# Optimization experiments

Hardware: AMD Instinct MI355X
Metric: run time of the kernel (lower is better)

Reference implementation:

```python
import jax, jax.numpy as jnp
import numpy as np

B, T, C = 2, 2048, 1024
H = 16
D = C // H  # head_dim = 64
EPS = 1e-06
MAX_SEQ = 2048


def make_rotary(dim, max_seq_len, base=10000):
    inv_freq = 1.0 / (base ** (jnp.arange(0, dim, 2, dtype=jnp.float32) / dim))
    pos = jnp.arange(max_seq_len, dtype=jnp.float32)
    sinusoid = jnp.einsum('i,j->ij', pos, inv_freq)  # (S, dim//2)
    return jnp.sin(sinusoid), jnp.cos(sinusoid)


def apply_rotary(x, sin, cos):
    # x: (B, T, H, D); sin/cos: (MAX_SEQ, D//2)
    t = x.shape[1]
    s = sin[:t][:, None, :]  # (T,1,D//2) broadcasts over B and H
    c = cos[:t][:, None, :]
    d = x.shape[-1]
    x1, x2 = x[..., :d // 2], x[..., d // 2:]
    return jnp.concatenate([x1 * c - x2 * s, x2 * c + x1 * s], axis=-1)


def yat_dense(x, kernel, bias, alpha, eps=EPS):
    # Yat layer: squared dot product over squared euclidean distance.
    dot = x @ kernel                                   # (..., out)
    x_sq = jnp.sum(x * x, axis=-1, keepdims=True)      # (..., 1)
    k_sq = jnp.sum(kernel * kernel, axis=0)            # (out,)
    dist = x_sq + k_sq - 2.0 * dot
    y = (dot * dot) / (dist + eps)
    out_f = kernel.shape[1]
    scale = (jnp.sqrt(jnp.float32(out_f)) / jnp.log(1.0 + jnp.float32(out_f))) ** alpha
    return y * scale + bias


def setup_inputs() -> dict:
    key = jax.random.key(0)
    ks = jax.random.split(key, 7)
    x = jax.random.normal(ks[0], (B, T, C), dtype=jnp.float32)
    mask = jnp.tril(jnp.ones((T, T), dtype=bool))[None].repeat(B, axis=0)  # (B,T,T) causal
    s = 1.0 / np.sqrt(C)
    w_attn = jax.random.normal(ks[1], (C, 3 * C), dtype=jnp.float32) * s
    b_attn = jnp.zeros((3 * C,), dtype=jnp.float32)
    a_attn = jnp.ones((1,), dtype=jnp.float32)
    w_proj = jax.random.normal(ks[2], (C, C), dtype=jnp.float32) * s
    b_proj = jnp.zeros((C,), dtype=jnp.float32)
    a_proj = jnp.ones((1,), dtype=jnp.float32)
    return {"x": x, "mask": mask, "w_attn": w_attn, "b_attn": b_attn,
            "a_attn": a_attn, "w_proj": w_proj, "b_proj": b_proj, "a_proj": a_proj}


def reference(x, mask, w_attn, b_attn, a_attn, w_proj, b_proj, a_proj):
    b, t, c = x.shape
    sin, cos = make_rotary(D, MAX_SEQ)
    qkv = yat_dense(x, w_attn, b_attn, a_attn)          # (B,T,3C)
    qkv = qkv.reshape(b, t, 3, H, D)
    q, k, v = jnp.moveaxis(qkv, 2, 0)                   # each (B,T,H,D)
    q = apply_rotary(q, sin, cos)
    k = apply_rotary(k, sin, cos)
    # heads-major layout for attention
    q = q.transpose(0, 2, 1, 3)                          # (B,H,T,D)
    k = k.transpose(0, 2, 1, 3)
    v = v.transpose(0, 2, 1, 3)
    scale = jnp.sqrt(jnp.float32(D))
    attn = jnp.einsum('bhqd,bhkd->bhqk', q, k) / scale   # (B,H,T,T)
    m = mask[:, None, :, :]                              # (B,1,T,T)
    attn = jnp.where(m, attn, jnp.finfo(jnp.float32).min)
    attn = jax.nn.softmax(attn, axis=-1)
    # dropout is identity in deterministic/eval mode
    out = jnp.einsum('bhqk,bhkd->bhqd', attn, v)         # (B,H,T,D)
    out = out.transpose(0, 2, 1, 3).reshape(b, t, c)     # (B,T,C)
    out = yat_dense(out, w_proj, b_proj, a_proj)
    return out
```

## Files before the change

### kernel.cpp

```cpp
#include <hip/hip_runtime.h>
#include <math.h>

#define TSEQ  2048
#define BATCH 2
#define NH    16
#define HD    64
#define CDIM  1024
#define N3C   3072
#define EPSY  1e-6f

typedef unsigned short u16;
typedef unsigned int u32;
typedef __attribute__((ext_vector_type(8))) short bf16x8;
typedef __attribute__((ext_vector_type(4))) float f32x4;

#define MFMA16(a, b, c) __builtin_amdgcn_mfma_f32_16x16x32_bf16(a, b, c, 0, 0, 0)

__device__ __forceinline__ u16 f2bf(float f) {
    unsigned u = __float_as_uint(f);
    return (u16)((u + 0x7fffu + ((u >> 16) & 1u)) >> 16);
}
__device__ __forceinline__ float bf2f(u16 h) {
    return __uint_as_float(((unsigned)h) << 16);
}
__device__ __forceinline__ void gload16(const void* g, void* l) {
    __builtin_amdgcn_global_load_lds(
        (const __attribute__((address_space(1))) unsigned int*)g,
        (__attribute__((address_space(3))) unsigned int*)l, 16, 0, 0);
}

__global__ void rope_init(float2* __restrict__ sc) {
    int idx = blockIdx.x * 256 + threadIdx.x;
    int t = idx >> 5, j = idx & 31;
    float inv = exp2f(-(float)j * 0.4152410118609203f);
    float ang = (float)t * inv;
    sc[idx] = make_float2(cosf(ang), sinf(ang));
}

__global__ void colsq_kernel(const float* __restrict__ wa,
                             const float* __restrict__ wp,
                             float* __restrict__ ks) {
    int bid = blockIdx.x, tid = threadIdx.x;
    int c = tid & 63, kq = tid >> 6;
    const float* W; int N, col, outoff;
    if (bid < 48) { W = wa; N = N3C;  col = bid * 64 + c;        outoff = 0;   }
    else          { W = wp; N = CDIM; col = (bid - 48) * 64 + c; outoff = N3C; }
    float s = 0.f;
    int i0 = kq * 256;
    #pragma unroll 4
    for (int i = i0; i < i0 + 256; ++i) {
        float v = W[(size_t)i * N + col];
        s = fmaf(v, v, s);
    }
    __shared__ float red[256];
    red[tid] = s;
    __syncthreads();
    if (kq == 0) ks[outoff + col] = red[c] + red[64 + c] + red[128 + c] + red[192 + c];
}

__global__ void convert_rows(const float* __restrict__ X, u16* __restrict__ Xhi,
                             float* __restrict__ rsq) {
    int row = blockIdx.x, tid = threadIdx.x;
    int lane = tid & 63, wv = tid >> 6;
    size_t base = (size_t)row * CDIM + tid * 4;
    float4 v = *(const float4*)(X + base);
    ushort4 hi;
    hi.x = f2bf(v.x); hi.y = f2bf(v.y); hi.z = f2bf(v.z); hi.w = f2bf(v.w);
    *(ushort4*)(Xhi + base) = hi;
    float s = v.x * v.x + v.y * v.y + v.z * v.z + v.w * v.w;
    #pragma unroll
    for (int off = 32; off; off >>= 1) s += __shfl_down(s, off, 64);
    __shared__ float red[4];
    if (lane == 0) red[wv] = s;
    __syncthreads();
    if (tid == 0) rsq[row] = red[0] + red[1] + red[2] + red[3];
}

__global__ void convert_wT(const float* __restrict__ W, u16* __restrict__ Whi,
                           int K, int N) {
    __shared__ float tile[64][68];
    int k0 = blockIdx.y * 64, n0 = blockIdx.x * 64;
    int tid = threadIdx.x;
    int r = tid >> 4, c4 = (tid & 15) * 4;
    #pragma unroll
    for (int i = 0; i < 4; ++i) {
        int k = k0 + r + i * 16;
        float4 v = *(const float4*)(W + (size_t)k * N + n0 + c4);
        *(float4*)&tile[r + i * 16][c4] = v;
    }
    __syncthreads();
    int n = tid >> 4, k4 = (tid & 15) * 4;
    #pragma unroll
    for (int i = 0; i < 4; ++i) {
        int nn = n + i * 16;
        ushort4 hi;
        hi.x = f2bf(tile[k4 + 0][nn]);
        hi.y = f2bf(tile[k4 + 1][nn]);
        hi.z = f2bf(tile[k4 + 2][nn]);
        hi.w = f2bf(tile[k4 + 3][nn]);
        *(ushort4*)(Whi + (size_t)(n0 + nn) * K + k0 + k4) = hi;
    }
}

__global__ __launch_bounds__(256, 4) void gemm1_fused(
    const u16* __restrict__ Ah, const u16* __restrict__ Bh,
    const float* __restrict__ bias, const float* __restrict__ rowsq,
    const float* __restrict__ colsq, const float* __restrict__ alphap,
    const float2* __restrict__ ropeSC,
    u16* __restrict__ Qb, u16* __restrict__ Kb, u16* __restrict__ Vt) {
    constexpr int BK = 32;
    const int K = CDIM;
    __shared__ u16 Ash[128 * BK], Bsh[128 * BK];
    int tid = threadIdx.x;
    int lane = tid & 63, wv = tid >> 6;
    int quad = lane >> 4, l15 = lane & 15;
    int wr = wv >> 1, wc = wv & 1;
    int bm = blockIdx.y * 128, bn = blockIdx.x * 128;
    int rsub = lane >> 2;
    int lc8 = (lane & 3) * 8;
    int gc8 = (((lane & 3) - (rsub >> 1)) & 3) * 8;
    int pf8 = ((quad + (l15 >> 1)) & 3) * 8;

    f32x4 acc[4][4];
    #pragma unroll
    for (int i = 0; i < 4; ++i)
        #pragma unroll
        for (int j = 0; j < 4; ++j) acc[i][j] = (f32x4){0.f, 0.f, 0.f, 0.f};

    for (int kt = 0; kt < K; kt += BK) {
        #pragma unroll
        for (int i = 0; i < 2; ++i) {
            int r = i * 64 + wv * 16 + rsub;
            gload16(Ah + (size_t)(bm + r) * K + kt + gc8, &Ash[r * BK + lc8]);
            gload16(Bh + (size_t)(bn + r) * K + kt + gc8, &Bsh[r * BK + lc8]);
        }
        __syncthreads();
        bf16x8 fah[4], fbh[4];
        #pragma unroll
        for (int i = 0; i < 4; ++i)
            fah[i] = *(const bf16x8*)&Ash[(wr * 64 + i * 16 + l15) * BK + pf8];
        #pragma unroll
        for (int j = 0; j < 4; ++j)
            fbh[j] = *(const bf16x8*)&Bsh[(wc * 64 + j * 16 + l15) * BK + pf8];
        #pragma unroll
        for (int i = 0; i < 4; ++i)
            #pragma unroll
            for (int j = 0; j < 4; ++j)
                acc[i][j] = MFMA16(fah[i], fbh[j], acc[i][j]);
        __syncthreads();
    }

    float alpha = alphap[0];
    float scale = powf(sqrtf((float)N3C) / logf(1.0f + (float)N3C), alpha);
    int segc0 = bn + wc * 64;
    int seg = segc0 >> 10;
    int h = (segc0 >> 6) & 15;
    int bglob = bm >> 11;
    int bh = bglob * NH + h;

    if (seg < 2) {
        u16* dst = (seg == 0) ? Qb : Kb;
        float qs = (seg == 0) ? 0.125f : 1.0f;
        #pragma unroll
        for (int i = 0; i < 4; ++i) {
            int tb = bm + wr * 64 + i * 16 + quad * 4;
            #pragma unroll
            for (int r = 0; r < 4; ++r) {
                int row = tb + r;
                int t = row & (TSEQ - 1);
                float rs = rowsq[row];
                float y[4];
                #pragma unroll
                for (int j = 0; j < 4; ++j) {
                    int col = segc0 + j * 16 + l15;
                    float dot = acc[i][j][r];
                    float dist = rs + colsq[col] - 2.0f * dot + EPSY;
                    y[j] = dot * dot / dist * scale + bias[col];
                }
                float2 sc0 = ropeSC[t * 32 + l15];
                float2 sc1 = ropeSC[t * 32 + 16 + l15];
                float c0 = sc0.x, s0 = sc0.y, c1 = sc1.x, s1 = sc1.y;
                size_t ob = ((size_t)bh * TSEQ + t) * HD;
                dst[ob + l15]      = f2bf((y[0] * c0 - y[2] * s0) * qs);
                dst[ob + 16 + l15] = f2bf((y[1] * c1 - y[3] * s1) * qs);
                dst[ob + 32 + l15] = f2bf((y[2] * c0 + y[0] * s0) * qs);
                dst[ob + 48 + l15] = f2bf((y[3] * c1 + y[1] * s1) * qs);
            }
        }
    } else {
        #pragma unroll
        for (int i = 0; i < 4; ++i) {
            int tb = bm + wr * 64 + i * 16 + quad * 4;
            int t0 = tb & (TSEQ - 1);
            #pragma unroll
            for (int j = 0; j < 4; ++j) {
                int col = segc0 + j * 16 + l15;
                int d = j * 16 + l15;
                float cs = colsq[col], bi = bias[col];
                ushort4 pk;
                u16* pp = (u16*)&pk;
                #pragma unroll
                for (int r = 0; r < 4; ++r) {
                    float dot = acc[i][j][r];
                    float dist = rowsq[tb + r] + cs - 2.0f * dot + EPSY;
                    pp[r] = f2bf(dot * dot / dist * scale + bi);
                }
                *(ushort4*)(Vt + ((size_t)bh * HD + d) * TSEQ + t0) = pk;
            }
        }
    }
}

__global__ __launch_bounds__(256, 4) void gemm_yat_mfma(
    const u16* __restrict__ Ah, const u16* __restrict__ Bh,
    const float* __restrict__ bias, const float* __restrict__ rowsq,
    const float* __restrict__ colsq, const float* __restrict__ alphap,
    float* __restrict__ outp, int M, int N, int K, float outf) {
    constexpr int BM = 128, BN = 64, BK = 32;
    __shared__ u16 Ash[BM * BK], Bsh[BN * BK];
    int tid = threadIdx.x;
    int lane = tid & 63, wv = tid >> 6;
    int quad = lane >> 4, l15 = lane & 15;
    int bm = blockIdx.y * BM, bn = blockIdx.x * BN;
    int rsub = lane >> 2;
    int lc8 = (lane & 3) * 8;
    int gc8 = (((lane & 3) - (rsub >> 1)) & 3) * 8;
    int pf8 = ((quad + (l15 >> 1)) & 3) * 8;

    f32x4 acc[2][4];
    #pragma unroll
    for (int i = 0; i < 2; ++i)
        #pragma unroll
        for (int j = 0; j < 4; ++j) acc[i][j] = (f32x4){0.f, 0.f, 0.f, 0.f};

    for (int kt = 0; kt < K; kt += BK) {
        #pragma unroll
        for (int i = 0; i < 2; ++i) {
            int r = i * 64 + wv * 16 + rsub;
            gload16(Ah + (size_t)(bm + r) * K + kt + gc8, &Ash[r * BK + lc8]);
        }
        {
            int r = wv * 16 + rsub;
            gload16(Bh + (size_t)(bn + r) * K + kt + gc8, &Bsh[r * BK + lc8]);
        }
        __syncthreads();
        bf16x8 fah[2], fbh[4];
        #pragma unroll
        for (int i = 0; i < 2; ++i)
            fah[i] = *(const bf16x8*)&Ash[(wv * 32 + i * 16 + l15) * BK + pf8];
        #pragma unroll
        for (int j = 0; j < 4; ++j)
            fbh[j] = *(const bf16x8*)&Bsh[(j * 16 + l15) * BK + pf8];
        #pragma unroll
        for (int i = 0; i < 2; ++i)
            #pragma unroll
            for (int j = 0; j < 4; ++j)
                acc[i][j] = MFMA16(fah[i], fbh[j], acc[i][j]);
        __syncthreads();
    }

    float alpha = alphap[0];
    float scale = powf(sqrtf(outf) / logf(1.0f + outf), alpha);
    #pragma unroll
    for (int j = 0; j < 4; ++j) {
        int col = bn + j * 16 + l15;
        float cs = colsq[col], bi = bias[col];
        #pragma unroll
        for (int i = 0; i < 2; ++i) {
            #pragma unroll
            for (int r = 0; r < 4; ++r) {
                int row = bm + wv * 32 + i * 16 + quad * 4 + r;
                float dot = acc[i][j][r];
                float dist = rowsq[row] + cs - 2.0f * dot + EPSY;
                outp[(size_t)row * N + col] = dot * dot / dist * scale + bi;
            }
        }
    }
}

__global__ __launch_bounds__(256) void attn_mfma(
    const u16* __restrict__ Qb, const u16* __restrict__ Kb,
    const u16* __restrict__ Vt, float* __restrict__ ctx) {
    __shared__ u16 Ksh[64 * 64];
    __shared__ u16 Vsh[64 * 64];
    int tid = threadIdx.x;
    int lane = tid & 63, wv = tid >> 6;
    int quad = lane >> 4, l15 = lane & 15;
    int bh = blockIdx.y;
    int b = bh >> 4, h = bh & 15;
    const u16* Qh = Qb + (size_t)bh * TSEQ * HD;
    const u16* Kh = Kb + (size_t)bh * TSEQ * HD;
    const u16* Vh = Vt + (size_t)bh * HD * TSEQ;
    const f32x4 zf = {0.f, 0.f, 0.f, 0.f};

    for (int pass = 0; pass < 2; ++pass) {
        int qb = pass ? (31 - blockIdx.x) : blockIdx.x;
        int qw = qb * 64 + wv * 16;
        bf16x8 bq0 = *(const bf16x8*)(Qh + (size_t)(qw + l15) * HD + quad * 8);
        bf16x8 bq1 = *(const bf16x8*)(Qh + (size_t)(qw + l15) * HD + 32 + quad * 8);

        f32x4 o[4] = {zf, zf, zf, zf};
        float l = 0.f;

        for (int kt = 0; kt <= qb; ++kt) {
            int k0 = kt * 64;
            __syncthreads();
            #pragma unroll
            for (int p = 0; p < 2; ++p) {
                int lin = p * 256 + tid;
                int rowi = lin >> 3, ch = lin & 7;
                int gk = (ch + rowi) & 7;
                gload16(Kh + (size_t)(k0 + rowi) * HD + gk * 8, &Ksh[lin * 8]);
                gload16(Vh + (size_t)rowi * TSEQ + k0 + gk * 8, &Vsh[lin * 8]);
            }
            __syncthreads();

            f32x4 st[4];
            #pragma unroll
            for (int mt = 0; mt < 4; ++mt) {
                int key = mt * 16 + l15;
                bf16x8 a0 = *(const bf16x8*)&Ksh[key * 64 + ((quad - key) & 7) * 8];
                bf16x8 a1 = *(const bf16x8*)&Ksh[key * 64 + ((4 + quad - key) & 7) * 8];
                st[mt] = MFMA16(a0, bq0, zf);
                st[mt] = MFMA16(a1, bq1, st[mt]);
            }
            if (kt == qb) {
                int q = qw + l15;
                #pragma unroll
                for (int mt = 0; mt < 4; ++mt)
                    #pragma unroll
                    for (int r = 0; r < 4; ++r)
                        if (k0 + mt * 16 + quad * 4 + r > q) st[mt][r] = -1e30f;
            }
            u32 pp[4][2];
            #pragma unroll
            for (int mt = 0; mt < 4; ++mt) {
                float p0 = __expf(st[mt][0]);
                float p1 = __expf(st[mt][1]);
                float p2 = __expf(st[mt][2]);
                float p3 = __expf(st[mt][3]);
                l += (p0 + p1) + (p2 + p3);
                pp[mt][0] = (u32)f2bf(p0) | ((u32)f2bf(p1) << 16);
                pp[mt][1] = (u32)f2bf(p2) | ((u32)f2bf(p3) << 16);
            }
            #pragma unroll
            for (int s = 0; s < 2; ++s) {
                u32 bw[4];
                #pragma unroll
                for (int w = 0; w < 4; ++w) {
                    int srcl = (((quad & 1) * 2 + (w >> 1)) << 4) + l15;
                    u32 vlo = (u32)__shfl((int)pp[2 * s][w & 1], srcl, 64);
                    u32 vhi = (u32)__shfl((int)pp[2 * s + 1][w & 1], srcl, 64);
                    bw[w] = (quad & 2) ? vhi : vlo;
                }
                bf16x8 bfr;
                *(u32*)&((short*)&bfr)[0] = bw[0];
                *(u32*)&((short*)&bfr)[2] = bw[1];
                *(u32*)&((short*)&bfr)[4] = bw[2];
                *(u32*)&((short*)&bfr)[6] = bw[3];
                #pragma unroll
                for (int dt = 0; dt < 4; ++dt) {
                    int d = dt * 16 + l15;
                    bf16x8 av = *(const bf16x8*)&Vsh[d * 64 + ((s * 4 + quad - d) & 7) * 8];
                    o[dt] = MFMA16(av, bfr, o[dt]);
                }
            }
        }

        l += __shfl_xor(l, 16, 64);
        l += __shfl_xor(l, 32, 64);
        float inv = 1.0f / l;
        #pragma unroll
        for (int dt = 0; dt < 4; ++dt) {
            float4 r;
            r.x = o[dt][0] * inv; r.y = o[dt][1] * inv;
            r.z = o[dt][2] * inv; r.w = o[dt][3] * inv;
            *(float4*)(ctx + ((size_t)b * TSEQ + qw + l15) * CDIM
                       + h * HD + dt * 16 + quad * 4) = r;
        }
    }
}

extern "C" void kernel_launch(void* const* d_in, const int* in_sizes, int n_in,
                              void* d_out, int out_size, void* d_ws, size_t ws_size,
                              hipStream_t stream) {
    const float* x      = (const float*)d_in[0];
    const float* w_attn = (const float*)d_in[2];
    const float* b_attn = (const float*)d_in[3];
    const float* a_attn = (const float*)d_in[4];
    const float* w_proj = (const float*)d_in[5];
    const float* b_proj = (const float*)d_in[6];
    const float* a_proj = (const float*)d_in[7];
    float* outp = (float*)d_out;

    char* ws = (char*)d_ws;
    float* ksq = (float*)(ws);
    float* xsq = (float*)(ws + 16384);
    float* osq = (float*)(ws + 32768);
    char* pA  = ws + 65536;
    u16* Ahi = (u16*)pA;
    float* ctx = (float*)pA;
    char* pWt = pA + 16777216;
    u16* Wthi = (u16*)pWt;
    char* pWp = pWt + 6291456;
    u16* Wphi = (u16*)pWp;
    char* pQ = pWp + 2097152;
    u16* Qb = (u16*)pQ;
    u16* Kb = (u16*)(pQ + 8388608);
    u16* Vt = (u16*)(pQ + 16777216);
    u16* Chi = (u16*)pQ;
    float2* ropeSC = (float2*)(pQ + 25165824);

    rope_init<<<256, 256, 0, stream>>>(ropeSC);
    colsq_kernel<<<64, 256, 0, stream>>>(w_attn, w_proj, ksq);
    convert_rows<<<BATCH * TSEQ, 256, 0, stream>>>(x, Ahi, xsq);
    convert_wT<<<dim3(N3C / 64, CDIM / 64), 256, 0, stream>>>(w_attn, Wthi, CDIM, N3C);
    convert_wT<<<dim3(CDIM / 64, CDIM / 64), 256, 0, stream>>>(w_proj, Wphi, CDIM, CDIM);
    gemm1_fused<<<dim3(N3C / 128, (BATCH * TSEQ) / 128), 256, 0, stream>>>(
        Ahi, Wthi, b_attn, xsq, ksq, a_attn, ropeSC, Qb, Kb, Vt);
    attn_mfma<<<dim3(16, BATCH * NH), 256, 0, stream>>>(Qb, Kb, Vt, ctx);
    convert_rows<<<BATCH * TSEQ, 256, 0, stream>>>(ctx, Chi, osq);
    gemm_yat_mfma<<<dim3(CDIM / 64, (BATCH * TSEQ) / 128), 256, 0, stream>>>(
        Chi, Wphi, b_proj, osq, ksq + N3C, a_proj, outp,
        BATCH * TSEQ, CDIM, CDIM, (float)CDIM);
}
```

Before: 270.0 us.

## Fuse context bf16 conversion and row-norm into attention epilogue; one q-block per CTA

```diff
diff --git a/kernel.cpp b/kernel.cpp
--- a/kernel.cpp
+++ b/kernel.cpp
@@ -29,8 +29,9 @@
         (__attribute__((address_space(3))) unsigned int*)l, 16, 0, 0);
 }
 
-__global__ void rope_init(float2* __restrict__ sc) {
+__global__ void rope_init(float2* __restrict__ sc, float* __restrict__ osq) {
     int idx = blockIdx.x * 256 + threadIdx.x;
+    if (idx < BATCH * TSEQ) osq[idx] = 0.f;
     int t = idx >> 5, j = idx & 31;
     float inv = exp2f(-(float)j * 0.4152410118609203f);
     float ang = (float)t * inv;
@@ -280,105 +281,110 @@
 
 __global__ __launch_bounds__(256) void attn_mfma(
     const u16* __restrict__ Qb, const u16* __restrict__ Kb,
-    const u16* __restrict__ Vt, float* __restrict__ ctx) {
+    const u16* __restrict__ Vt, u16* __restrict__ Chi,
+    float* __restrict__ osq) {
     __shared__ u16 Ksh[64 * 64];
     __shared__ u16 Vsh[64 * 64];
     int tid = threadIdx.x;
     int lane = tid & 63, wv = tid >> 6;
     int quad = lane >> 4, l15 = lane & 15;
-    int bh = blockIdx.y;
+    int bh = blockIdx.x;
     int b = bh >> 4, h = bh & 15;
     const u16* Qh = Qb + (size_t)bh * TSEQ * HD;
     const u16* Kh = Kb + (size_t)bh * TSEQ * HD;
     const u16* Vh = Vt + (size_t)bh * HD * TSEQ;
     const f32x4 zf = {0.f, 0.f, 0.f, 0.f};
 
-    for (int pass = 0; pass < 2; ++pass) {
-        int qb = pass ? (31 - blockIdx.x) : blockIdx.x;
-        int qw = qb * 64 + wv * 16;
-        bf16x8 bq0 = *(const bf16x8*)(Qh + (size_t)(qw + l15) * HD + quad * 8);
-        bf16x8 bq1 = *(const bf16x8*)(Qh + (size_t)(qw + l15) * HD + 32 + quad * 8);
-
-        f32x4 o[4] = {zf, zf, zf, zf};
-        float l = 0.f;
-
-        for (int kt = 0; kt <= qb; ++kt) {
-            int k0 = kt * 64;
-            __syncthreads();
-            #pragma unroll
-            for (int p = 0; p < 2; ++p) {
-                int lin = p * 256 + tid;
-                int rowi = lin >> 3, ch = lin & 7;
-                int gk = (ch + rowi) & 7;
-                gload16(Kh + (size_t)(k0 + rowi) * HD + gk * 8, &Ksh[lin * 8]);
-                gload16(Vh + (size_t)rowi * TSEQ + k0 + gk * 8, &Vsh[lin * 8]);
+    int qb = 31 - blockIdx.y;
+    int qw = qb * 64 + wv * 16;
+    bf16x8 bq0 = *(const bf16x8*)(Qh + (size_t)(qw + l15) * HD + quad * 8);
+    bf16x8 bq1 = *(const bf16x8*)(Qh + (size_t)(qw + l15) * HD + 32 + quad * 8);
+
+    f32x4 o[4] = {zf, zf, zf, zf};
+    float l = 0.f;
+
+    for (int kt = 0; kt <= qb; ++kt) {
+        int k0 = kt * 64;
+        __syncthreads();
+        #pragma unroll
+        for (int p = 0; p < 2; ++p) {
+            int lin = p * 256 + tid;
+            int rowi = lin >> 3, ch = lin & 7;
+            int gk = (ch + rowi) & 7;
+            gload16(Kh + (size_t)(k0 + rowi) * HD + gk * 8, &Ksh[lin * 8]);
+            gload16(Vh + (size_t)rowi * TSEQ + k0 + gk * 8, &Vsh[lin * 8]);
+        }
+        __syncthreads();
+
+        f32x4 st[4];
+        #pragma unroll
+        for (int mt = 0; mt < 4; ++mt) {
+            int key = mt * 16 + l15;
+            bf16x8 a0 = *(const bf16x8*)&Ksh[key * 64 + ((quad - key) & 7) * 8];
+            bf16x8 a1 = *(const bf16x8*)&Ksh[key * 64 + ((4 + quad - key) & 7) * 8];
+            st[mt] = MFMA16(a0, bq0, zf);
+            st[mt] = MFMA16(a1, bq1, st[mt]);
+        }
+        if (kt == qb) {
+            int q = qw + l15;
+            #pragma unroll
+            for (int mt = 0; mt < 4; ++mt)
+                #pragma unroll
+                for (int r = 0; r < 4; ++r)
+                    if (k0 + mt * 16 + quad * 4 + r > q) st[mt][r] = -1e30f;
+        }
+        u32 pp[4][2];
+        #pragma unroll
+        for (int mt = 0; mt < 4; ++mt) {
+            float p0 = __expf(st[mt][0]);
+            float p1 = __expf(st[mt][1]);
+            float p2 = __expf(st[mt][2]);
+            float p3 = __expf(st[mt][3]);
+            l += (p0 + p1) + (p2 + p3);
+            pp[mt][0] = (u32)f2bf(p0) | ((u32)f2bf(p1) << 16);
+            pp[mt][1] = (u32)f2bf(p2) | ((u32)f2bf(p3) << 16);
+        }
+        #pragma unroll
+        for (int s = 0; s < 2; ++s) {
+            u32 bw[4];
+            #pragma unroll
+            for (int w = 0; w < 4; ++w) {
+                int srcl = (((quad & 1) * 2 + (w >> 1)) << 4) + l15;
+                u32 vlo = (u32)__shfl((int)pp[2 * s][w & 1], srcl, 64);
+                u32 vhi = (u32)__shfl((int)pp[2 * s + 1][w & 1], srcl, 64);
+                bw[w] = (quad & 2) ? vhi : vlo;
             }
-            __syncthreads();
-
-            f32x4 st[4];
-            #pragma unroll
-            for (int mt = 0; mt < 4; ++mt) {
-                int key = mt * 16 + l15;
-                bf16x8 a0 = *(const bf16x8*)&Ksh[key * 64 + ((quad - key) & 7) * 8];
-                bf16x8 a1 = *(const bf16x8*)&Ksh[key * 64 + ((4 + quad - key) & 7) * 8];
-                st[mt] = MFMA16(a0, bq0, zf);
-                st[mt] = MFMA16(a1, bq1, st[mt]);
+            bf16x8 bfr;
+            *(u32*)&((short*)&bfr)[0] = bw[0];
+            *(u32*)&((short*)&bfr)[2] = bw[1];
+            *(u32*)&((short*)&bfr)[4] = bw[2];
+            *(u32*)&((short*)&bfr)[6] = bw[3];
+            #pragma unroll
+            for (int dt = 0; dt < 4; ++dt) {
+                int d = dt * 16 + l15;
+                bf16x8 av = *(const bf16x8*)&Vsh[d * 64 + ((s * 4 + quad - d) & 7) * 8];
+                o[dt] = MFMA16(av, bfr, o[dt]);
             }
-            if (kt == qb) {
-                int q = qw + l15;
-                #pragma unroll
-                for (int mt = 0; mt < 4; ++mt)
-                    #pragma unroll
-                    for (int r = 0; r < 4; ++r)
-                        if (k0 + mt * 16 + quad * 4 + r > q) st[mt][r] = -1e30f;
-            }
-            u32 pp[4][2];
-            #pragma unroll
-            for (int mt = 0; mt < 4; ++mt) {
-                float p0 = __expf(st[mt][0]);
-                float p1 = __expf(st[mt][1]);
-                float p2 = __expf(st[mt][2]);
-                float p3 = __expf(st[mt][3]);
-                l += (p0 + p1) + (p2 + p3);
-                pp[mt][0] = (u32)f2bf(p0) | ((u32)f2bf(p1) << 16);
-                pp[mt][1] = (u32)f2bf(p2) | ((u32)f2bf(p3) << 16);
-            }
-            #pragma unroll
-            for (int s = 0; s < 2; ++s) {
-                u32 bw[4];
-                #pragma unroll
-                for (int w = 0; w < 4; ++w) {
-                    int srcl = (((quad & 1) * 2 + (w >> 1)) << 4) + l15;
-                    u32 vlo = (u32)__shfl((int)pp[2 * s][w & 1], srcl, 64);
-                    u32 vhi = (u32)__shfl((int)pp[2 * s + 1][w & 1], srcl, 64);
-                    bw[w] = (quad & 2) ? vhi : vlo;
-                }
-                bf16x8 bfr;
-                *(u32*)&((short*)&bfr)[0] = bw[0];
-                *(u32*)&((short*)&bfr)[2] = bw[1];
-                *(u32*)&((short*)&bfr)[4] = bw[2];
-                *(u32*)&((short*)&bfr)[6] = bw[3];
-                #pragma unroll
-                for (int dt = 0; dt < 4; ++dt) {
-                    int d = dt * 16 + l15;
-                    bf16x8 av = *(const bf16x8*)&Vsh[d * 64 + ((s * 4 + quad - d) & 7) * 8];
-                    o[dt] = MFMA16(av, bfr, o[dt]);
-                }
-            }
-        }
-
-        l += __shfl_xor(l, 16, 64);
-        l += __shfl_xor(l, 32, 64);
-        float inv = 1.0f / l;
-        #pragma unroll
-        for (int dt = 0; dt < 4; ++dt) {
-            float4 r;
-            r.x = o[dt][0] * inv; r.y = o[dt][1] * inv;
-            r.z = o[dt][2] * inv; r.w = o[dt][3] * inv;
-            *(float4*)(ctx + ((size_t)b * TSEQ + qw + l15) * CDIM
-                       + h * HD + dt * 16 + quad * 4) = r;
-        }
-    }
+        }
+    }
+
+    l += __shfl_xor(l, 16, 64);
+    l += __shfl_xor(l, 32, 64);
+    float inv = 1.0f / l;
+    int row = (b << 11) + qw + l15;
+    float ss = 0.f;
+    #pragma unroll
+    for (int dt = 0; dt < 4; ++dt) {
+        float v0 = o[dt][0] * inv, v1 = o[dt][1] * inv;
+        float v2 = o[dt][2] * inv, v3 = o[dt][3] * inv;
+        ss += v0 * v0 + v1 * v1 + v2 * v2 + v3 * v3;
+        ushort4 pk;
+        pk.x = f2bf(v0); pk.y = f2bf(v1); pk.z = f2bf(v2); pk.w = f2bf(v3);
+        *(ushort4*)(Chi + (size_t)row * CDIM + h * HD + dt * 16 + quad * 4) = pk;
+    }
+    ss += __shfl_xor(ss, 16, 64);
+    ss += __shfl_xor(ss, 32, 64);
+    if (quad == 0) atomicAdd(osq + row, ss);
 }
 
 extern "C" void kernel_launch(void* const* d_in, const int* in_sizes, int n_in,
@@ -399,7 +405,7 @@
     float* osq = (float*)(ws + 32768);
     char* pA  = ws + 65536;
     u16* Ahi = (u16*)pA;
-    float* ctx = (float*)pA;
+    u16* Chi = (u16*)pA;
     char* pWt = pA + 16777216;
     u16* Wthi = (u16*)pWt;
     char* pWp = pWt + 6291456;
@@ -408,18 +414,16 @@
     u16* Qb = (u16*)pQ;
     u16* Kb = (u16*)(pQ + 8388608);
     u16* Vt = (u16*)(pQ + 16777216);
-    u16* Chi = (u16*)pQ;
     float2* ropeSC = (float2*)(pQ + 25165824);
 
-    rope_init<<<256, 256, 0, stream>>>(ropeSC);
+    rope_init<<<256, 256, 0, stream>>>(ropeSC, osq);
     colsq_kernel<<<64, 256, 0, stream>>>(w_attn, w_proj, ksq);
     convert_rows<<<BATCH * TSEQ, 256, 0, stream>>>(x, Ahi, xsq);
     convert_wT<<<dim3(N3C / 64, CDIM / 64), 256, 0, stream>>>(w_attn, Wthi, CDIM, N3C);
     convert_wT<<<dim3(CDIM / 64, CDIM / 64), 256, 0, stream>>>(w_proj, Wphi, CDIM, CDIM);
     gemm1_fused<<<dim3(N3C / 128, (BATCH * TSEQ) / 128), 256, 0, stream>>>(
         Ahi, Wthi, b_attn, xsq, ksq, a_attn, ropeSC, Qb, Kb, Vt);
-    attn_mfma<<<dim3(16, BATCH * NH), 256, 0, stream>>>(Qb, Kb, Vt, ctx);
-    convert_rows<<<BATCH * TSEQ, 256, 0, stream>>>(ctx, Chi, osq);
+    attn_mfma<<<dim3(BATCH * NH, 32), 256, 0, stream>>>(Qb, Kb, Vt, Chi, osq);
     gemm_yat_mfma<<<dim3(CDIM / 64, (BATCH * TSEQ) / 128), 256, 0, stream>>>(
         Chi, Wphi, b_proj, osq, ksq + N3C, a_proj, outp,
         BATCH * TSEQ, CDIM, CDIM, (float)CDIM);
```

After: 248.8 us. -7.8%, faster.
